# Kernel optimization log

Hardware: AMD Instinct MI355X
Metric: run time of the kernel (lower is better)

The kernel has to match this reference:

```python
import jax, jax.numpy as jnp
import numpy as np

VOCAB = 16000
DIM = 1024
B, T = 4, 2048


def setup_inputs() -> dict:
    key = jax.random.key(0)
    k_ids, k_emb, k_w, k_lw, k_lb = jax.random.split(key, 5)
    input_ids = jax.random.randint(k_ids, (B, T), 0, VOCAB)
    embed = jax.random.normal(k_emb, (VOCAB, DIM), dtype=jnp.float32)
    # w_state = I + 0.05 * (default Linear init ~ U(-1/sqrt(dim), 1/sqrt(dim)))
    bound = 1.0 / np.sqrt(DIM)
    w_state = jnp.eye(DIM, dtype=jnp.float32) + 0.05 * jax.random.uniform(
        k_w, (DIM, DIM), minval=-bound, maxval=bound, dtype=jnp.float32)
    lm_w = jax.random.uniform(k_lw, (VOCAB, DIM), minval=-bound, maxval=bound, dtype=jnp.float32)
    lm_b = jax.random.uniform(k_lb, (VOCAB,), minval=-bound, maxval=bound, dtype=jnp.float32)
    return {"input_ids": input_ids, "embed": embed, "w_state": w_state,
            "lm_w": lm_w, "lm_b": lm_b}


def reference(input_ids, embed, w_state, lm_w, lm_b):
    # h: [B, T, D]
    h = embed[input_ids]
    state0 = jnp.zeros((h.shape[0], h.shape[2]), dtype=h.dtype)

    def step(state, h_t):
        # nn.Linear: state @ W^T ; then add input injection
        new_state = state @ w_state.T + h_t
        return new_state, new_state

    # scan over time: inputs [T, B, D]
    _, outs = jax.lax.scan(step, state0, jnp.swapaxes(h, 0, 1))
    hidden = jnp.swapaxes(outs, 0, 1)  # [B, T, D]
    logits = hidden @ lm_w.T + lm_b    # [B, T, V]
    return logits
```

## Files before the change

kernel.cpp:

```cpp
#include <hip/hip_runtime.h>
#include <hip/hip_bf16.h>
#include <stdint.h>

#define DD 1024
#define BB 4
#define TT 2048
#define VV 16000
#define LCH 8
#define NR 1024
#define PADR 512
#define NPAD 16128
#define M1C ((size_t)DD * DD)

typedef __bf16 bf16_t;
typedef float f32x4_t __attribute__((ext_vector_type(4)));
typedef bf16_t bf16x8_t __attribute__((ext_vector_type(8)));
typedef bf16_t bf16x4_t __attribute__((ext_vector_type(4)));

#define KIND_SQ 0
#define KIND_ROUND 1
#define KIND_LEVEL 2
#define KIND_CARRY 3

__device__ __forceinline__ void gload16(const void* g, void* l) {
  __builtin_amdgcn_global_load_lds((const __attribute__((address_space(1))) void*)g,
                                   (__attribute__((address_space(3))) void*)l, 16, 0, 0);
}

__global__ __launch_bounds__(256) void k_cvt(const float* __restrict__ src,
                                             bf16_t* __restrict__ dst, int n4) {
  int i = blockIdx.x * blockDim.x + threadIdx.x;
  int stride = gridDim.x * blockDim.x;
  for (; i < n4; i += stride) {
    float4 v = ((const float4*)src)[i];
    union { ushort4 u; bf16_t h[4]; } p;
    p.h[0] = (bf16_t)v.x; p.h[1] = (bf16_t)v.y;
    p.h[2] = (bf16_t)v.z; p.h[3] = (bf16_t)v.w;
    ((ushort4*)dst)[i] = p.u;
  }
}

struct JobF {
  const float* A; const float* B; float* C; const float* Cin;
  int kind; int dlt;
};
struct JobsF { JobF j[8]; };

__global__ __launch_bounds__(256) void k_gatherF(const float* __restrict__ embed,
                                                 const int* __restrict__ ids,
                                                 float* __restrict__ slab0) {
  int r = blockIdx.x;
  int b = r & 3, c = r >> 2;
  int id = ids[b * TT + c * LCH];
  const float4* s = (const float4*)(embed + (size_t)id * DD);
  float4* d = (float4*)(slab0 + (size_t)r * DD);
  for (int i = threadIdx.x; i < DD / 4; i += blockDim.x) d[i] = s[i];
}

template <int NS>
__device__ __forceinline__ void swrite(char* base, int byteoff, float4 v) {
  float r0 = v.x, r1 = v.y, r2 = v.z, r3 = v.w;
#pragma unroll
  for (int p = 0; p < NS; ++p) {
    bf16x4_t h;
    h[0] = (bf16_t)r0; h[1] = (bf16_t)r1; h[2] = (bf16_t)r2; h[3] = (bf16_t)r3;
    *(bf16x4_t*)(base + p * 5120 + byteoff) = h;
    if (p + 1 < NS) {
      r0 -= (float)h[0]; r1 -= (float)h[1]; r2 -= (float)h[2]; r3 -= (float)h[3];
    }
  }
}

template <int NS, bool NN, int MODE>
__device__ __forceinline__ void mbodyF(bf16_t* __restrict__ SBb, const JobF& jb,
                                       const float* __restrict__ embed,
                                       const int* __restrict__ ids,
                                       bf16_t* __restrict__ hidden) {
  const float* A = jb.A;
  const float* Bm = jb.B;
  const int tid = threadIdx.x, lane = tid & 63, wave = tid >> 6;
  const int i0 = blockIdx.y * 64, j0 = blockIdx.x * 64;
  const int wm = (wave >> 1) * 32, wn = (wave & 1) * 32;
  char* Ap = (char*)SBb;
  char* Bp = Ap + NS * 5120;
  const int arow = tid >> 2;
  const int akb = (tid & 3) * 8;
  const int bj = tid & 63, bk4 = (tid >> 6) * 4;
  const int frow = lane & 15, fkb = (lane >> 4) * 16;
  f32x4_t acc[2][2] = {};

  const float* Aptr = A + (size_t)(i0 + arow) * DD + (tid & 3) * 4;
  const float* BptrNT = Bm + (size_t)(j0 + arow) * DD + (tid & 3) * 4;
  const float* BptrNN = Bm + (size_t)bk4 * DD + j0 + bj;

  float4 a0 = *(const float4*)(Aptr);
  float4 a1 = *(const float4*)(Aptr + 16);
  float4 b0, b1;
  float s0[4], s1[4];
  if (!NN) {
    b0 = *(const float4*)(BptrNT);
    b1 = *(const float4*)(BptrNT + 16);
  } else {
#pragma unroll
    for (int s = 0; s < 4; ++s) s0[s] = BptrNN[(size_t)s * DD];
#pragma unroll
    for (int s = 0; s < 4; ++s) s1[s] = BptrNN[(size_t)(16 + s) * DD];
  }

  for (int k0 = 0;;) {
    __syncthreads();
    swrite<NS>(Ap, arow * 80 + akb, a0);
    swrite<NS>(Ap, arow * 80 + akb + 32, a1);
    if (!NN) {
      swrite<NS>(Bp, arow * 80 + akb, b0);
      swrite<NS>(Bp, arow * 80 + akb + 32, b1);
    } else {
      float4 t0; t0.x = s0[0]; t0.y = s0[1]; t0.z = s0[2]; t0.w = s0[3];
      float4 t1; t1.x = s1[0]; t1.y = s1[1]; t1.z = s1[2]; t1.w = s1[3];
      swrite<NS>(Bp, bj * 80 + bk4 * 2, t0);
      swrite<NS>(Bp, bj * 80 + bk4 * 2 + 32, t1);
    }
    __syncthreads();
    int kn = k0 + 32;
    if (kn < DD) {
      a0 = *(const float4*)(Aptr + kn);
      a1 = *(const float4*)(Aptr + kn + 16);
      if (!NN) {
        b0 = *(const float4*)(BptrNT + kn);
        b1 = *(const float4*)(BptrNT + kn + 16);
      } else {
#pragma unroll
        for (int s = 0; s < 4; ++s) s0[s] = BptrNN[(size_t)(kn + s) * DD];
#pragma unroll
        for (int s = 0; s < 4; ++s) s1[s] = BptrNN[(size_t)(kn + 16 + s) * DD];
      }
    }
    bf16x8_t af[NS][2], bfx[NS][2];
#pragma unroll
    for (int p = 0; p < NS; ++p)
#pragma unroll
      for (int mf = 0; mf < 2; ++mf) {
        af[p][mf] = *(const bf16x8_t*)(Ap + p * 5120 + (wm + mf * 16 + frow) * 80 + fkb);
        bfx[p][mf] = *(const bf16x8_t*)(Bp + p * 5120 + (wn + mf * 16 + frow) * 80 + fkb);
      }
#pragma unroll
    for (int pa = 0; pa < NS; ++pa)
#pragma unroll
      for (int pb = 0; pb < NS; ++pb) {
        if (pa + pb < NS) {
#pragma unroll
          for (int mf = 0; mf < 2; ++mf)
#pragma unroll
            for (int nf = 0; nf < 2; ++nf)
              acc[mf][nf] = __builtin_amdgcn_mfma_f32_16x16x32_bf16(
                  af[pa][mf], bfx[pb][nf], acc[mf][nf], 0, 0, 0);
        }
      }
    k0 = kn;
    if (k0 >= DD) break;
  }

  const int ecol = lane & 15, er4 = (lane >> 4) * 4;
#pragma unroll
  for (int mf = 0; mf < 2; ++mf) {
#pragma unroll
    for (int nf = 0; nf < 2; ++nf) {
      const int rb = i0 + wm + mf * 16 + er4;
      const int cj = j0 + wn + nf * 16 + ecol;
#pragma unroll
      for (int rg = 0; rg < 4; ++rg) {
        const int ri = rb + rg;
        float v = acc[mf][nf][rg];
        if (MODE == 0) {
          jb.C[(size_t)ri * DD + cj] = v;
        } else if (MODE == 1) {
          int b = ri & 3, c = ri >> 2, t = c * LCH + jb.dlt;
          v += embed[(size_t)ids[b * TT + t] * DD + cj];
          jb.C[(size_t)ri * DD + cj] = v;
        } else if (MODE == 2) {
          v += jb.Cin[(size_t)ri * DD + cj];
          jb.C[(size_t)ri * DD + cj] = v;
        } else {
          int b = ri & 3, c = ri >> 2, t = c * LCH + jb.dlt;
          hidden[((size_t)b * TT + t) * DD + cj] =
              (bf16_t)(v + jb.Cin[(size_t)ri * DD + cj]);
        }
      }
    }
  }
}

__global__ __launch_bounds__(256, 2) void k_multiF(JobsF jobs,
                                                   const float* __restrict__ embed,
                                                   const int* __restrict__ ids,
                                                   bf16_t* __restrict__ hidden) {
  __shared__ __align__(16) bf16_t SBb[6 * 2560];
  const JobF& jb = jobs.j[blockIdx.z];
  if (jb.kind == KIND_SQ)
    mbodyF<3, true, 0>(SBb, jb, embed, ids, hidden);
  else if (jb.kind == KIND_ROUND)
    mbodyF<2, false, 1>(SBb, jb, embed, ids, hidden);
  else if (jb.kind == KIND_LEVEL)
    mbodyF<2, false, 2>(SBb, jb, embed, ids, hidden);
  else
    mbodyF<2, false, 3>(SBb, jb, embed, ids, hidden);
}

#define NTK 32

__global__ __launch_bounds__(512, 2) void k_lmhead2(
    const bf16_t* __restrict__ Ah, const bf16_t* __restrict__ Bw,
    const float* __restrict__ bias, float* __restrict__ Cout) {
  __shared__ __align__(16) char LB[4 * 32768];
  const int tid = threadIdx.x, lane = tid & 63, wave = tid >> 6;
  const int wr = wave >> 2, wc = wave & 3;
  int orig = blockIdx.y * gridDim.x + blockIdx.x;
  int swz = (orig & 7) * 252 + (orig >> 3);
  int by = swz / 63, bx = swz % 63;
  const int m0 = by * 256, n0 = bx * 256;

  const int srow = tid >> 2;
  const int scb = (tid & 3) * 16;

  auto stage = [&](int t) {
    char* buf = LB + (size_t)(t & 3) * 32768;
#pragma unroll
    for (int p = 0; p < 2; ++p) {
      int row = p * 128 + srow;
      int sw = ((row >> 1) & 3) << 4;
      gload16((const char*)Ah + ((size_t)(m0 + row) * DD + t * 32) * 2 + (scb ^ sw),
              buf + p * 8192 + wave * 1024);
      gload16((const char*)Bw + ((size_t)(n0 + row) * DD + t * 32) * 2 + (scb ^ sw),
              buf + 16384 + p * 8192 + wave * 1024);
    }
  };

  const int frow = lane & 15;
  const int c4b = (lane >> 4) * 16;
  f32x4_t acc[8][4] = {};

  stage(0); stage(1); stage(2);
  asm volatile("s_waitcnt vmcnt(8)\ns_barrier" ::: "memory");

  for (int t = 0; t < NTK; ++t) {
    char* Abuf = LB + (size_t)(t & 3) * 32768;
    char* Bbuf = Abuf + 16384;
    if (t + 3 < NTK) stage(t + 3);
    bf16x8_t afr[4], bfr[4];
#pragma unroll
    for (int nf = 0; nf < 4; ++nf) {
      int r = wc * 64 + nf * 16 + frow;
      bfr[nf] = *(const bf16x8_t*)(Bbuf + r * 64 + (c4b ^ (((r >> 1) & 3) << 4)));
    }
#pragma unroll
    for (int mf = 0; mf < 4; ++mf) {
      int r = wr * 128 + mf * 16 + frow;
      afr[mf] = *(const bf16x8_t*)(Abuf + r * 64 + (c4b ^ (((r >> 1) & 3) << 4)));
    }
    __builtin_amdgcn_s_setprio(1);
#pragma unroll
    for (int mf = 0; mf < 4; ++mf)
#pragma unroll
      for (int nf = 0; nf < 4; ++nf)
        acc[mf][nf] = __builtin_amdgcn_mfma_f32_16x16x32_bf16(
            afr[mf], bfr[nf], acc[mf][nf], 0, 0, 0);
    __builtin_amdgcn_s_setprio(0);
#pragma unroll
    for (int mf = 0; mf < 4; ++mf) {
      int r = wr * 128 + 64 + mf * 16 + frow;
      afr[mf] = *(const bf16x8_t*)(Abuf + r * 64 + (c4b ^ (((r >> 1) & 3) << 4)));
    }
    __builtin_amdgcn_s_setprio(1);
#pragma unroll
    for (int mf = 0; mf < 4; ++mf)
#pragma unroll
      for (int nf = 0; nf < 4; ++nf)
        acc[4 + mf][nf] = __builtin_amdgcn_mfma_f32_16x16x32_bf16(
            afr[mf], bfr[nf], acc[4 + mf][nf], 0, 0, 0);
    __builtin_amdgcn_s_setprio(0);
    if (t < NTK - 3) {
      asm volatile("s_waitcnt vmcnt(8)\ns_barrier" ::: "memory");
    } else if (t == NTK - 3) {
      asm volatile("s_waitcnt vmcnt(4)\ns_barrier" ::: "memory");
    } else if (t == NTK - 2) {
      asm volatile("s_waitcnt vmcnt(0)\ns_barrier" ::: "memory");
    }
  }

  const int ecol = lane & 15, er4 = (lane >> 4) * 4;
#pragma unroll
  for (int mf = 0; mf < 8; ++mf) {
#pragma unroll
    for (int nf = 0; nf < 4; ++nf) {
      int gm = m0 + wr * 128 + mf * 16 + er4;
      int gn = n0 + wc * 64 + nf * 16 + ecol;
      if (gn < VV) {
        float bv = bias[gn];
#pragma unroll
        for (int rg = 0; rg < 4; ++rg)
          Cout[(size_t)(gm + rg) * VV + gn] = acc[mf][nf][rg] + bv;
      }
    }
  }
}

extern "C" void kernel_launch(void* const* d_in, const int* in_sizes, int n_in,
                              void* d_out, int out_size, void* d_ws, size_t ws_size,
                              hipStream_t stream) {
  (void)in_sizes; (void)n_in; (void)out_size; (void)ws_size;
  const int* ids = (const int*)d_in[0];
  const float* embed = (const float*)d_in[1];
  const float* w_state = (const float*)d_in[2];
  const float* lm_w = (const float*)d_in[3];
  const float* lm_b = (const float*)d_in[4];
  float* out = (float*)d_out;

  const size_t M1 = M1C;
  float* PW = (float*)d_ws;
  float* Q = PW + 8 * M1;
  float* LOC = Q + 7 * M1;
  float* E0 = LOC + 8 * M1;
  float* E1 = E0 + (size_t)(PADR + NR) * DD;
  bf16_t* HID = (bf16_t*)(E1 + (size_t)(PADR + NR) * DD);
  bf16_t* LWB = HID + (size_t)BB * TT * DD;
  float* E0d = E0 + (size_t)PADR * DD;
  float* E1d = E1 + (size_t)PADR * DD;

  k_cvt<<<2048, 256, 0, stream>>>(lm_w, LWB, VV * DD / 4);
  hipMemsetAsync(LWB + (size_t)VV * DD, 0,
                 (size_t)(NPAD - VV) * DD * sizeof(bf16_t), stream);
  hipMemcpyAsync(PW, w_state, M1 * sizeof(float), hipMemcpyDeviceToDevice, stream);
  k_gatherF<<<NR, 256, 0, stream>>>(embed, ids, LOC);
  hipMemsetAsync(E0, 0, (size_t)PADR * DD * sizeof(float), stream);
  hipMemsetAsync(E1, 0, (size_t)PADR * DD * sizeof(float), stream);

  JobsF J{};
  J.j[0] = JobF{w_state, w_state, PW + M1, nullptr, KIND_SQ, 0};
  J.j[1] = JobF{LOC, w_state, LOC + M1, nullptr, KIND_ROUND, 1};
  k_multiF<<<dim3(16, 16, 2), 256, 0, stream>>>(J, embed, ids, HID);
  J.j[0] = JobF{PW + M1, w_state, PW + 2 * M1, nullptr, KIND_SQ, 0};
  J.j[1] = JobF{PW + M1, PW + M1, PW + 3 * M1, nullptr, KIND_SQ, 0};
  J.j[2] = JobF{LOC + M1, w_state, LOC + 2 * M1, nullptr, KIND_ROUND, 2};
  k_multiF<<<dim3(16, 16, 3), 256, 0, stream>>>(J, embed, ids, HID);
  J.j[0] = JobF{PW + 3 * M1, w_state, PW + 4 * M1, nullptr, KIND_SQ, 0};
  J.j[1] = JobF{PW + 3 * M1, PW + M1, PW + 5 * M1, nullptr, KIND_SQ, 0};
  J.j[2] = JobF{PW + 3 * M1, PW + 2 * M1, PW + 6 * M1, nullptr, KIND_SQ, 0};
  J.j[3] = JobF{PW + 3 * M1, PW + 3 * M1, PW + 7 * M1, nullptr, KIND_SQ, 0};
  J.j[4] = JobF{LOC + 2 * M1, w_state, LOC + 3 * M1, nullptr, KIND_ROUND, 3};
  k_multiF<<<dim3(16, 16, 5), 256, 0, stream>>>(J, embed, ids, HID);
  for (int d = 4; d <= 7; ++d) {
    const float* src = (d == 4) ? (PW + 7 * M1) : (Q + (size_t)(d - 5) * M1);
    J.j[0] = JobF{src, src, Q + (size_t)(d - 4) * M1, nullptr, KIND_SQ, 0};
    J.j[1] = JobF{LOC + (size_t)(d - 1) * M1, w_state, LOC + (size_t)d * M1,
                  nullptr, KIND_ROUND, d};
    k_multiF<<<dim3(16, 16, 2), 256, 0, stream>>>(J, embed, ids, HID);
  }
  hipMemcpyAsync(E0d, LOC + 7 * M1, M1 * sizeof(float),
                 hipMemcpyDeviceToDevice, stream);

  float* inp = E0d;
  float* outp = E1d;
  for (int k = 0; k < 8; ++k) {
    JobsF J2{};
    int nz = 0;
    if (k <= 2) {
      const float* src = Q + (size_t)(k + 3) * M1;
      J2.j[nz++] = JobF{src, src, Q + (size_t)(k + 4) * M1, nullptr, KIND_SQ, 0};
    }
    const float* Bq = (k == 0) ? (PW + 7 * M1) : (Q + (size_t)(k - 1) * M1);
    J2.j[nz++] = JobF{inp - (size_t)(4 << k) * DD, Bq, outp, inp, KIND_LEVEL, 0};
    k_multiF<<<dim3(16, 16, nz), 256, 0, stream>>>(J2, embed, ids, HID);
    float* t = inp; inp = outp; outp = t;
  }

  JobsF Jc{};
  for (int d = 0; d < 8; ++d)
    Jc.j[d] = JobF{inp - (size_t)4 * DD, PW + (size_t)d * M1, nullptr,
                   LOC + (size_t)d * M1, KIND_CARRY, d};
  k_multiF<<<dim3(16, 16, 8), 256, 0, stream>>>(Jc, embed, ids, HID);

  dim3 gl(NPAD / 256, (BB * TT) / 256);
  k_lmhead2<<<gl, 512, 0, stream>>>(HID, LWB, lm_b, out);
}
```

Before: 902.3 us.

## Halve local chunk length and rebalance parallel-scan power schedule

Changes the linear-recurrence decomposition from chunks of 8 steps to chunks of 4, doubling the number of chunk rows. Fewer local sequential rounds and fewer W powers are needed before the cross-chunk scan, but the scan gains a level and each round-type job now covers twice as many rows (grid y doubled, with square-power jobs early-exiting the extra blocks). The aim is a shorter serial dependency chain of kernel launches at the cost of more row work per level.

```diff
diff --git a/kernel.cpp b/kernel.cpp
--- a/kernel.cpp
+++ b/kernel.cpp
@@ -6,9 +6,9 @@
 #define BB 4
 #define TT 2048
 #define VV 16000
-#define LCH 8
-#define NR 1024
-#define PADR 512
+#define LCH 4
+#define NR 2048
+#define PADR 1024
 #define NPAD 16128
 #define M1C ((size_t)DD * DD)
 
@@ -196,9 +196,10 @@
                                                    bf16_t* __restrict__ hidden) {
   __shared__ __align__(16) bf16_t SBb[6 * 2560];
   const JobF& jb = jobs.j[blockIdx.z];
-  if (jb.kind == KIND_SQ)
+  if (jb.kind == KIND_SQ) {
+    if (blockIdx.y >= 16) return;
     mbodyF<3, true, 0>(SBb, jb, embed, ids, hidden);
-  else if (jb.kind == KIND_ROUND)
+  } else if (jb.kind == KIND_ROUND)
     mbodyF<2, false, 1>(SBb, jb, embed, ids, hidden);
   else if (jb.kind == KIND_LEVEL)
     mbodyF<2, false, 2>(SBb, jb, embed, ids, hidden);
@@ -316,68 +317,57 @@
   float* out = (float*)d_out;
 
   const size_t M1 = M1C;
-  float* PW = (float*)d_ws;
-  float* Q = PW + 8 * M1;
-  float* LOC = Q + 7 * M1;
+  float* POW = (float*)d_ws;
+  float* LOC = POW + 11 * M1;
   float* E0 = LOC + 8 * M1;
-  float* E1 = E0 + (size_t)(PADR + NR) * DD;
-  bf16_t* HID = (bf16_t*)(E1 + (size_t)(PADR + NR) * DD);
-  bf16_t* LWB = HID + (size_t)BB * TT * DD;
+  float* E1 = E0 + 3 * M1;
+  bf16_t* HID = (bf16_t*)(E1 + 3 * M1);
+  bf16_t* LWB = HID + 8 * M1;
   float* E0d = E0 + (size_t)PADR * DD;
   float* E1d = E1 + (size_t)PADR * DD;
 
   k_cvt<<<2048, 256, 0, stream>>>(lm_w, LWB, VV * DD / 4);
   hipMemsetAsync(LWB + (size_t)VV * DD, 0,
                  (size_t)(NPAD - VV) * DD * sizeof(bf16_t), stream);
-  hipMemcpyAsync(PW, w_state, M1 * sizeof(float), hipMemcpyDeviceToDevice, stream);
   k_gatherF<<<NR, 256, 0, stream>>>(embed, ids, LOC);
   hipMemsetAsync(E0, 0, (size_t)PADR * DD * sizeof(float), stream);
   hipMemsetAsync(E1, 0, (size_t)PADR * DD * sizeof(float), stream);
 
   JobsF J{};
-  J.j[0] = JobF{w_state, w_state, PW + M1, nullptr, KIND_SQ, 0};
-  J.j[1] = JobF{LOC, w_state, LOC + M1, nullptr, KIND_ROUND, 1};
-  k_multiF<<<dim3(16, 16, 2), 256, 0, stream>>>(J, embed, ids, HID);
-  J.j[0] = JobF{PW + M1, w_state, PW + 2 * M1, nullptr, KIND_SQ, 0};
-  J.j[1] = JobF{PW + M1, PW + M1, PW + 3 * M1, nullptr, KIND_SQ, 0};
-  J.j[2] = JobF{LOC + M1, w_state, LOC + 2 * M1, nullptr, KIND_ROUND, 2};
-  k_multiF<<<dim3(16, 16, 3), 256, 0, stream>>>(J, embed, ids, HID);
-  J.j[0] = JobF{PW + 3 * M1, w_state, PW + 4 * M1, nullptr, KIND_SQ, 0};
-  J.j[1] = JobF{PW + 3 * M1, PW + M1, PW + 5 * M1, nullptr, KIND_SQ, 0};
-  J.j[2] = JobF{PW + 3 * M1, PW + 2 * M1, PW + 6 * M1, nullptr, KIND_SQ, 0};
-  J.j[3] = JobF{PW + 3 * M1, PW + 3 * M1, PW + 7 * M1, nullptr, KIND_SQ, 0};
-  J.j[4] = JobF{LOC + 2 * M1, w_state, LOC + 3 * M1, nullptr, KIND_ROUND, 3};
-  k_multiF<<<dim3(16, 16, 5), 256, 0, stream>>>(J, embed, ids, HID);
-  for (int d = 4; d <= 7; ++d) {
-    const float* src = (d == 4) ? (PW + 7 * M1) : (Q + (size_t)(d - 5) * M1);
-    J.j[0] = JobF{src, src, Q + (size_t)(d - 4) * M1, nullptr, KIND_SQ, 0};
-    J.j[1] = JobF{LOC + (size_t)(d - 1) * M1, w_state, LOC + (size_t)d * M1,
-                  nullptr, KIND_ROUND, d};
-    k_multiF<<<dim3(16, 16, 2), 256, 0, stream>>>(J, embed, ids, HID);
-  }
-  hipMemcpyAsync(E0d, LOC + 7 * M1, M1 * sizeof(float),
+  J.j[0] = JobF{w_state, w_state, POW, nullptr, KIND_SQ, 0};
+  J.j[1] = JobF{LOC, w_state, LOC + 2 * M1, nullptr, KIND_ROUND, 1};
+  k_multiF<<<dim3(16, 32, 2), 256, 0, stream>>>(J, embed, ids, HID);
+  J.j[0] = JobF{POW, w_state, POW + M1, nullptr, KIND_SQ, 0};
+  J.j[1] = JobF{POW, POW, POW + 2 * M1, nullptr, KIND_SQ, 0};
+  J.j[2] = JobF{LOC + 2 * M1, w_state, LOC + 4 * M1, nullptr, KIND_ROUND, 2};
+  k_multiF<<<dim3(16, 32, 3), 256, 0, stream>>>(J, embed, ids, HID);
+  J.j[0] = JobF{POW + 2 * M1, POW + 2 * M1, POW + 3 * M1, nullptr, KIND_SQ, 0};
+  J.j[1] = JobF{LOC + 4 * M1, w_state, LOC + 6 * M1, nullptr, KIND_ROUND, 3};
+  k_multiF<<<dim3(16, 32, 2), 256, 0, stream>>>(J, embed, ids, HID);
+
+  hipMemcpyAsync(E0d, LOC + 6 * M1, 2 * M1 * sizeof(float),
                  hipMemcpyDeviceToDevice, stream);
 
   float* inp = E0d;
   float* outp = E1d;
-  for (int k = 0; k < 8; ++k) {
+  for (int k = 0; k < 9; ++k) {
     JobsF J2{};
     int nz = 0;
-    if (k <= 2) {
-      const float* src = Q + (size_t)(k + 3) * M1;
-      J2.j[nz++] = JobF{src, src, Q + (size_t)(k + 4) * M1, nullptr, KIND_SQ, 0};
-    }
-    const float* Bq = (k == 0) ? (PW + 7 * M1) : (Q + (size_t)(k - 1) * M1);
-    J2.j[nz++] = JobF{inp - (size_t)(4 << k) * DD, Bq, outp, inp, KIND_LEVEL, 0};
-    k_multiF<<<dim3(16, 16, nz), 256, 0, stream>>>(J2, embed, ids, HID);
+    J2.j[nz++] = JobF{inp - (size_t)(4 << k) * DD, POW + (size_t)(k + 2) * M1,
+                      outp, inp, KIND_LEVEL, 0};
+    if (k <= 6)
+      J2.j[nz++] = JobF{POW + (size_t)(k + 3) * M1, POW + (size_t)(k + 3) * M1,
+                        POW + (size_t)(k + 4) * M1, nullptr, KIND_SQ, 0};
+    k_multiF<<<dim3(16, 32, nz), 256, 0, stream>>>(J2, embed, ids, HID);
     float* t = inp; inp = outp; outp = t;
   }
 
   JobsF Jc{};
-  for (int d = 0; d < 8; ++d)
-    Jc.j[d] = JobF{inp - (size_t)4 * DD, PW + (size_t)d * M1, nullptr,
-                   LOC + (size_t)d * M1, KIND_CARRY, d};
-  k_multiF<<<dim3(16, 16, 8), 256, 0, stream>>>(Jc, embed, ids, HID);
+  Jc.j[0] = JobF{inp - (size_t)4 * DD, w_state, nullptr, LOC, KIND_CARRY, 0};
+  for (int d = 1; d < LCH; ++d)
+    Jc.j[d] = JobF{inp - (size_t)4 * DD, POW + (size_t)(d - 1) * M1, nullptr,
+                   LOC + (size_t)d * 2 * M1, KIND_CARRY, d};
+  k_multiF<<<dim3(16, 32, LCH), 256, 0, stream>>>(Jc, embed, ids, HID);
 
   dim3 gl(NPAD / 256, (BB * TT) / 256);
   k_lmhead2<<<gl, 512, 0, stream>>>(HID, LWB, lm_b, out);
```

Result: no change. 892.6 us (-1.1%).
